# Optimization experiments

Measured on AMD Instinct MI355X. Metric: run time of the kernel, lower is better.

## Reference

```python
import jax, jax.numpy as jnp
import numpy as np

NUM_STEPS = 5  # matches init num_steps
N_NODES = 500_000
N_EDGES = 32_000_000


def setup_inputs() -> dict:
    key = jax.random.key(0)
    k1, k2, k3 = jax.random.split(key, 3)
    prior_probs = jax.random.uniform(k1, (N_NODES,), dtype=jnp.float32)
    edge_index = jax.random.randint(k2, (2, N_EDGES), 0, N_NODES, dtype=jnp.int32)
    edge_probs = jax.random.uniform(k3, (N_EDGES,), dtype=jnp.float32)
    return {"prior_probs": prior_probs, "edge_index": edge_index, "edge_probs": edge_probs}


def reference(prior_probs, edge_index, edge_probs):
    num_nodes = prior_probs.shape[0]
    source = edge_index[0]
    target = edge_index[1]
    p_t_u = prior_probs
    prod_terms = jnp.ones_like(prior_probs)
    for _ in range(NUM_STEPS):
        # gather node activation at source, weight by edge prob, scatter-add into target
        message = edge_probs * p_t_u[source]            # [E]
        agg = jax.ops.segment_sum(message, target, num_segments=num_nodes)  # [N]
        delta = 1.0 - jnp.exp(-agg)
        new_p_t_u = prod_terms * delta
        prod_terms = prod_terms * (1.0 - new_p_t_u)
        p_t_u = new_p_t_u
    p_final = 1.0 - prod_terms + prior_probs
    return p_final.reshape(-1, 1)
```

## Files before the change

### kernel.cpp

```cpp
#include <hip/hip_runtime.h>
#include <hip/hip_fp16.h>

#define NUM_STEPS 5
typedef unsigned int u32;

#define RSH 10
#define RSZ 1024
#define SB  512
#define ST  512
#define SPLIT 2
#define SRC_BITS 19
#define SRC_MASK 0x7FFFFu

static inline size_t align256(size_t x){ return (x + 255) & ~(size_t)255; }


__global__ void init_fast(const float* __restrict__ prior, __half* __restrict__ p,
                          float* __restrict__ prod, int n){
    int i = blockIdx.x*blockDim.x + threadIdx.x;
    if(i<n){ p[i]=__float2half_rn(prior[i]); prod[i]=1.0f; }
}

__global__ void hist_kernel(const int* __restrict__ dst, long long E, int B,
                            u32* __restrict__ blk_cnt){
    extern __shared__ u32 hist[];
    int sb = blockIdx.x;
    long long E4 = E >> 2;
    long long chunk = (E4 + SB - 1)/SB;
    long long i0 = (long long)sb*chunk;
    long long i1 = i0 + chunk; if(i1 > E4) i1 = E4;
    for(int b=threadIdx.x; b<B; b+=blockDim.x) hist[b]=0;
    __syncthreads();
    const int4* d4 = (const int4*)dst;
    for(long long i=i0+threadIdx.x; i<i1; i+=blockDim.x){
        int4 d = d4[i];
        atomicAdd(&hist[((u32)d.x)>>RSH], 1u);
        atomicAdd(&hist[((u32)d.y)>>RSH], 1u);
        atomicAdd(&hist[((u32)d.z)>>RSH], 1u);
        atomicAdd(&hist[((u32)d.w)>>RSH], 1u);
    }
    if(sb==0){
        for(long long e=(E4<<2)+threadIdx.x; e<E; e+=blockDim.x)
            atomicAdd(&hist[((u32)dst[e])>>RSH], 1u);
    }
    __syncthreads();
    for(int b=threadIdx.x; b<B; b+=blockDim.x) blk_cnt[(size_t)sb*B + b] = hist[b];
}

__global__ void colscan_kernel(u32* __restrict__ blk_cnt, int B, u32* __restrict__ tot){
    __shared__ u32 s[SB];
    int b = blockIdx.x, t = threadIdx.x;
    u32 v = blk_cnt[(size_t)t*B + b];
    s[t] = v; __syncthreads();
    for(int off=1; off<SB; off<<=1){
        u32 x = (t>=off) ? s[t-off] : 0;
        __syncthreads();
        s[t] += x;
        __syncthreads();
    }
    blk_cnt[(size_t)t*B + b] = s[t] - v;
    if(t==SB-1) tot[b] = s[SB-1];
}

__global__ void basescan_kernel(const u32* __restrict__ tot, u32* __restrict__ base, int B){
    __shared__ u32 s[256];
    int t = threadIdx.x;
    u32 v0 = (2*t   < B) ? tot[2*t]   : 0;
    u32 v1 = (2*t+1 < B) ? tot[2*t+1] : 0;
    u32 sum = v0 + v1;
    s[t] = sum; __syncthreads();
    for(int off=1; off<256; off<<=1){
        u32 x = (t>=off) ? s[t-off] : 0;
        __syncthreads();
        s[t] += x;
        __syncthreads();
    }
    u32 run = s[t] - sum;
    if(2*t   < B) base[2*t]   = run;
    if(2*t+1 < B) base[2*t+1] = run + v0;
    if(t==255) base[B] = s[255];
}

__global__ void scatter_kernel(const int* __restrict__ src, const int* __restrict__ dst,
                               const float* __restrict__ ep, long long E, int B,
                               const u32* __restrict__ blk_rel, const u32* __restrict__ base,
                               uint2* __restrict__ edges){
    extern __shared__ u32 cur[];
    int sb = blockIdx.x;
    long long E4 = E >> 2;
    long long chunk = (E4 + SB - 1)/SB;
    long long i0 = (long long)sb*chunk;
    long long i1 = i0 + chunk; if(i1 > E4) i1 = E4;
    for(int b=threadIdx.x; b<B; b+=blockDim.x)
        cur[b] = base[b] + blk_rel[(size_t)sb*B + b];
    __syncthreads();
    const int4*   s4 = (const int4*)src;
    const int4*   d4 = (const int4*)dst;
    const float4* w4 = (const float4*)ep;
    for(long long i=i0+threadIdx.x; i<i1; i+=blockDim.x){
        int4 s = s4[i]; int4 d = d4[i]; float4 w = w4[i];
        u32 dd, pos;
        dd=(u32)d.x; pos=atomicAdd(&cur[dd>>RSH],1u);
        edges[pos]=make_uint2(((u32)s.x)|((dd&(RSZ-1))<<SRC_BITS), __float_as_uint(w.x));
        dd=(u32)d.y; pos=atomicAdd(&cur[dd>>RSH],1u);
        edges[pos]=make_uint2(((u32)s.y)|((dd&(RSZ-1))<<SRC_BITS), __float_as_uint(w.y));
        dd=(u32)d.z; pos=atomicAdd(&cur[dd>>RSH],1u);
        edges[pos]=make_uint2(((u32)s.z)|((dd&(RSZ-1))<<SRC_BITS), __float_as_uint(w.z));
        dd=(u32)d.w; pos=atomicAdd(&cur[dd>>RSH],1u);
        edges[pos]=make_uint2(((u32)s.w)|((dd&(RSZ-1))<<SRC_BITS), __float_as_uint(w.w));
    }
    if(sb==0){
        for(long long e=(E4<<2)+threadIdx.x; e<E; e+=blockDim.x){
            u32 dd=(u32)dst[e];
            u32 pos=atomicAdd(&cur[dd>>RSH],1u);
            edges[pos]=make_uint2(((u32)src[e])|((dd&(RSZ-1))<<SRC_BITS), __float_as_uint(ep[e]));
        }
    }
}

__global__ __launch_bounds__(512) void
step_kernel(const uint2* __restrict__ edges, const u32* __restrict__ base,
            const __half* __restrict__ p, float* __restrict__ pacc){
    __shared__ float acc[2][RSZ];
    int blk = blockIdx.x;
    int b   = blk >> 1;
    int part= blk & 1;
    int t   = threadIdx.x;
    for(int k=t; k<RSZ; k+=blockDim.x){ acc[0][k]=0.0f; acc[1][k]=0.0f; }
    __syncthreads();
    u32 e0 = base[b], e1 = base[b+1];
    u32 cnt = e1 - e0;
    u32 s0 = e0 + (cnt*part)/SPLIT;
    u32 s1 = e0 + (cnt*(part+1))/SPLIT;
    int rep = t & 1;
    for(u32 e = s0 + t; e < s1; e += blockDim.x){
        uint2 pk = edges[e];
        float pv = __half2float(p[pk.x & SRC_MASK]);
        atomicAdd(&acc[rep][pk.x >> SRC_BITS], __uint_as_float(pk.y) * pv);
    }
    __syncthreads();
    float* dstp = pacc + (size_t)blk * RSZ;
    for(int k=t; k<RSZ; k+=blockDim.x) dstp[k] = acc[0][k] + acc[1][k];
}

__global__ void combine_kernel(const float* __restrict__ pacc, __half* __restrict__ p,
                               float* __restrict__ prod, const float* __restrict__ prior,
                               float* __restrict__ out, int n, int final_step){
    int i = blockIdx.x*blockDim.x + threadIdx.x;
    if(i < n){
        int b = i >> RSH, k = i & (RSZ-1);
        float a = pacc[(size_t)(b*SPLIT    )*RSZ + k]
                + pacc[(size_t)(b*SPLIT + 1)*RSZ + k];
        float pr_old = prod[i];
        float np = pr_old * (1.0f - expf(-a));
        float pr = pr_old * (1.0f - np);
        prod[i] = pr;
        p[i] = __float2half_rn(np);
        if(final_step) out[i] = 1.0f - pr + prior[i];
    }
}


__global__ void init_kernel(const float* __restrict__ prior, float* __restrict__ p,
                            float* __restrict__ prod, float* __restrict__ agg, int n){
    int i = blockIdx.x*blockDim.x + threadIdx.x;
    if(i<n){ p[i]=prior[i]; prod[i]=1.0f; agg[i]=0.0f; }
}

__global__ void edge_kernel(const int* __restrict__ src, const int* __restrict__ dst,
                            const float* __restrict__ ep, const float* __restrict__ p,
                            float* __restrict__ agg, int e4, int e_rem, long long e4base){
    int i = blockIdx.x*blockDim.x + threadIdx.x;
    if(i < e4){
        int4   s = ((const int4*)src)[i];
        int4   t = ((const int4*)dst)[i];
        float4 w = ((const float4*)ep)[i];
        atomicAdd(&agg[t.x], w.x * p[s.x]);
        atomicAdd(&agg[t.y], w.y * p[s.y]);
        atomicAdd(&agg[t.z], w.z * p[s.z]);
        atomicAdd(&agg[t.w], w.w * p[s.w]);
    }
    if(blockIdx.x==0 && threadIdx.x < e_rem){
        long long e = e4base + threadIdx.x;
        atomicAdd(&agg[dst[e]], ep[e]*p[src[e]]);
    }
}

__global__ void node_kernel(float* __restrict__ p, float* __restrict__ prod,
                            float* __restrict__ agg, const float* __restrict__ prior,
                            float* __restrict__ out, int n, int final_step){
    int i = blockIdx.x*blockDim.x + threadIdx.x;
    if(i<n){
        float a = agg[i]; agg[i]=0.0f;
        float pr_old = prod[i];
        float np = pr_old*(1.0f - expf(-a));
        float pr = pr_old*(1.0f - np);
        prod[i]=pr; p[i]=np;
        if(final_step) out[i] = 1.0f - pr + prior[i];
    }
}


extern "C" void kernel_launch(void* const* d_in, const int* in_sizes, int n_in,
                              void* d_out, int out_size, void* d_ws, size_t ws_size,
                              hipStream_t stream){
    const float* prior = (const float*)d_in[0];
    const int*   eidx  = (const int*)d_in[1];
    const float* ep    = (const float*)d_in[2];

    const int n = in_sizes[0];
    const long long E = (long long)in_sizes[2];
    const int* src = eidx;
    const int* dst = eidx + E;
    float* out = (float*)d_out;

    const int B = (n + RSZ - 1) >> RSH;

    size_t szNh  = align256((size_t)n * 2);
    size_t szN   = align256((size_t)n * 4);
    size_t szB1  = align256((size_t)(B + 1) * 4);
    size_t szB   = align256((size_t)B * 4);
    size_t szCnt = align256((size_t)SB * B * 4);
    size_t szAcc = align256((size_t)SPLIT * B * RSZ * 4);
    size_t szE2  = align256((size_t)E * 8);

    size_t off_p    = 0;
    size_t off_prod = off_p + szNh;
    size_t off_base = off_prod + szN;
    size_t off_tot  = off_base + szB1;
    size_t off_cnt  = off_tot + szB;
    size_t off_acc  = off_cnt + szCnt;
    size_t off_edge = off_acc + szAcc;
    size_t need     = off_edge + szE2;

    char* ws = (char*)d_ws;

    if(ws_size >= need && n < (1 << SRC_BITS) && B <= 512){
        __half* p    = (__half*)(ws + off_p);
        float*  prod = (float*) (ws + off_prod);
        u32*    base = (u32*)   (ws + off_base);
        u32*    tot  = (u32*)   (ws + off_tot);
        u32*    cnt  = (u32*)   (ws + off_cnt);
        float*  pacc = (float*) (ws + off_acc);
        uint2*  edges= (uint2*) (ws + off_edge);

        const int nb_n = (n + 255)/256;
        init_fast<<<nb_n, 256, 0, stream>>>(prior, p, prod, n);
        hist_kernel<<<SB, ST, (size_t)B*4, stream>>>(dst, E, B, cnt);
        colscan_kernel<<<B, SB, 0, stream>>>(cnt, B, tot);
        basescan_kernel<<<1, 256, 0, stream>>>(tot, base, B);
        scatter_kernel<<<SB, ST, (size_t)B*4, stream>>>(src, dst, ep, E, B, cnt, base, edges);

        for(int step=0; step<NUM_STEPS; ++step){
            step_kernel<<<B*SPLIT, 512, 0, stream>>>(edges, base, p, pacc);
            combine_kernel<<<nb_n, 256, 0, stream>>>(pacc, p, prod, prior, out, n,
                                                     step == NUM_STEPS-1 ? 1 : 0);
        }
    } else {
        float* p    = (float*)d_ws;
        float* prod = p + n;
        float* agg  = prod + n;
        const int nb_n = (n + 255)/256;
        init_kernel<<<nb_n, 256, 0, stream>>>(prior, p, prod, agg, n);
        const int e4 = (int)(E/4);
        const int e_rem = (int)(E%4);
        const long long e4base = (long long)e4*4;
        const int nb_e = (e4 + 255)/256;
        for(int step=0; step<NUM_STEPS; ++step){
            edge_kernel<<<nb_e, 256, 0, stream>>>(src, dst, ep, p, agg, e4, e_rem, e4base);
            node_kernel<<<nb_n, 256, 0, stream>>>(p, prod, agg, prior, out, n,
                                                  step == NUM_STEPS-1 ? 1 : 0);
        }
    }
}
```

Baseline: 1.346 ms.

## Stage scatter writes through shared-memory bins and unroll step kernel edge loop

The scatter kernel now buffers up to eight edges per destination bucket in shared memory and flushes full bins as contiguous 64-byte runs, so most global writes land as grouped stores instead of scattered 8-byte ones. Overflow edges past the bin capacity are written directly at their final slot. The step kernel loop is unrolled by four so several edge loads and gathers can be in flight before the LDS atomics. In exchange the scatter adds three block barriers per iteration and a larger static shared-memory footprint, which may lower occupancy.

```diff
diff --git a/kernel.cpp b/kernel.cpp
--- a/kernel.cpp
+++ b/kernel.cpp
@@ -7,7 +7,10 @@
 #define RSH 10
 #define RSZ 1024
 #define SB  512
+#define HT  512
 #define ST  512
+#define NBMAX 512
+#define BINS 8
 #define SPLIT 2
 #define SRC_BITS 19
 #define SRC_MASK 0x7FFFFu
@@ -81,40 +84,79 @@
     if(t==255) base[B] = s[255];
 }
 
-__global__ void scatter_kernel(const int* __restrict__ src, const int* __restrict__ dst,
-                               const float* __restrict__ ep, long long E, int B,
-                               const u32* __restrict__ blk_rel, const u32* __restrict__ base,
-                               uint2* __restrict__ edges){
-    extern __shared__ u32 cur[];
-    int sb = blockIdx.x;
+__global__ __launch_bounds__(ST) void
+scatter_kernel(const int* __restrict__ src, const int* __restrict__ dst,
+               const float* __restrict__ ep, long long E, int B,
+               const u32* __restrict__ blk_rel, const u32* __restrict__ base,
+               uint2* __restrict__ edges){
+    __shared__ uint2 bin[NBMAX][BINS];
+    __shared__ u32 cnt[NBMAX];
+    __shared__ u32 gcur[NBMAX];
+    const int sb = blockIdx.x, t = threadIdx.x;
     long long E4 = E >> 2;
     long long chunk = (E4 + SB - 1)/SB;
     long long i0 = (long long)sb*chunk;
     long long i1 = i0 + chunk; if(i1 > E4) i1 = E4;
-    for(int b=threadIdx.x; b<B; b+=blockDim.x)
-        cur[b] = base[b] + blk_rel[(size_t)sb*B + b];
-    __syncthreads();
-    const int4*   s4 = (const int4*)src;
-    const int4*   d4 = (const int4*)dst;
-    const float4* w4 = (const float4*)ep;
-    for(long long i=i0+threadIdx.x; i<i1; i+=blockDim.x){
-        int4 s = s4[i]; int4 d = d4[i]; float4 w = w4[i];
-        u32 dd, pos;
-        dd=(u32)d.x; pos=atomicAdd(&cur[dd>>RSH],1u);
-        edges[pos]=make_uint2(((u32)s.x)|((dd&(RSZ-1))<<SRC_BITS), __float_as_uint(w.x));
-        dd=(u32)d.y; pos=atomicAdd(&cur[dd>>RSH],1u);
-        edges[pos]=make_uint2(((u32)s.y)|((dd&(RSZ-1))<<SRC_BITS), __float_as_uint(w.y));
-        dd=(u32)d.z; pos=atomicAdd(&cur[dd>>RSH],1u);
-        edges[pos]=make_uint2(((u32)s.z)|((dd&(RSZ-1))<<SRC_BITS), __float_as_uint(w.z));
-        dd=(u32)d.w; pos=atomicAdd(&cur[dd>>RSH],1u);
-        edges[pos]=make_uint2(((u32)s.w)|((dd&(RSZ-1))<<SRC_BITS), __float_as_uint(w.w));
+    for(int b=t; b<B; b+=ST){ cnt[b]=0; gcur[b]=base[b]+blk_rel[(size_t)sb*B+b]; }
+    __syncthreads();
+    const int4*   s4=(const int4*)src;
+    const int4*   d4=(const int4*)dst;
+    const float4* w4=(const float4*)ep;
+    for(long long it=i0; it<i1; it+=ST){
+        long long i = it + t;
+        bool valid = (i < i1);
+        u32 bk[4]; u32 sl[4]; uint2 pl[4];
+        if(valid){
+            int4 s=s4[i]; int4 d=d4[i]; float4 w=w4[i];
+            u32 dd;
+            dd=(u32)d.x; bk[0]=dd>>RSH; pl[0]=make_uint2(((u32)s.x)|((dd&(RSZ-1))<<SRC_BITS), __float_as_uint(w.x));
+            dd=(u32)d.y; bk[1]=dd>>RSH; pl[1]=make_uint2(((u32)s.y)|((dd&(RSZ-1))<<SRC_BITS), __float_as_uint(w.y));
+            dd=(u32)d.z; bk[2]=dd>>RSH; pl[2]=make_uint2(((u32)s.z)|((dd&(RSZ-1))<<SRC_BITS), __float_as_uint(w.z));
+            dd=(u32)d.w; bk[3]=dd>>RSH; pl[3]=make_uint2(((u32)s.w)|((dd&(RSZ-1))<<SRC_BITS), __float_as_uint(w.w));
+            #pragma unroll
+            for(int k=0;k<4;k++) sl[k]=atomicAdd(&cnt[bk[k]],1u);
+        }
+        __syncthreads();
+        if(valid){
+            #pragma unroll
+            for(int k=0;k<4;k++){
+                if(sl[k] < BINS) bin[bk[k]][sl[k]] = pl[k];
+                else             edges[gcur[bk[k]] + sl[k]] = pl[k];
+            }
+        }
+        __syncthreads();
+        for(int b=t; b<B; b+=ST){
+            u32 c = cnt[b];
+            if(c >= BINS){
+                u32 g = gcur[b];
+                #pragma unroll
+                for(int k2=0;k2<BINS;k2++) edges[g+k2] = bin[b][k2];
+                gcur[b] = g + c;
+                cnt[b]  = 0;
+            }
+        }
+        __syncthreads();
     }
     if(sb==0){
-        for(long long e=(E4<<2)+threadIdx.x; e<E; e+=blockDim.x){
-            u32 dd=(u32)dst[e];
-            u32 pos=atomicAdd(&cur[dd>>RSH],1u);
-            edges[pos]=make_uint2(((u32)src[e])|((dd&(RSZ-1))<<SRC_BITS), __float_as_uint(ep[e]));
-        }
+        long long tb = E4<<2;
+        int nt = (int)(E - tb);
+        if(nt > 0){
+            bool v = (t < nt);
+            u32 bk0=0, sl0=0; uint2 pl0=make_uint2(0,0);
+            if(v){
+                u32 dd=(u32)dst[tb+t]; bk0=dd>>RSH;
+                pl0=make_uint2(((u32)src[tb+t])|((dd&(RSZ-1))<<SRC_BITS), __float_as_uint(ep[tb+t]));
+                sl0=atomicAdd(&cnt[bk0],1u);
+            }
+            __syncthreads();
+            if(v){ if(sl0<BINS) bin[bk0][sl0]=pl0; else edges[gcur[bk0]+sl0]=pl0; }
+            __syncthreads();
+        }
+    }
+    for(int b=t; b<B; b+=ST){
+        u32 c = cnt[b]; if(c > BINS) c = BINS;
+        u32 g = gcur[b];
+        for(u32 k2=0;k2<c;k2++) edges[g+k2] = bin[b][k2];
     }
 }
 
@@ -126,21 +168,39 @@
     int b   = blk >> 1;
     int part= blk & 1;
     int t   = threadIdx.x;
-    for(int k=t; k<RSZ; k+=blockDim.x){ acc[0][k]=0.0f; acc[1][k]=0.0f; }
+    for(int k=t; k<RSZ; k+=512){ acc[0][k]=0.0f; acc[1][k]=0.0f; }
     __syncthreads();
     u32 e0 = base[b], e1 = base[b+1];
     u32 cnt = e1 - e0;
-    u32 s0 = e0 + (cnt*part)/SPLIT;
-    u32 s1 = e0 + (cnt*(part+1))/SPLIT;
+    u32 s0 = e0 + (cnt*(u32)part)/SPLIT;
+    u32 s1 = e0 + (cnt*(u32)(part+1))/SPLIT;
     int rep = t & 1;
-    for(u32 e = s0 + t; e < s1; e += blockDim.x){
-        uint2 pk = edges[e];
-        float pv = __half2float(p[pk.x & SRC_MASK]);
-        atomicAdd(&acc[rep][pk.x >> SRC_BITS], __uint_as_float(pk.y) * pv);
+    u32 n = s1 - s0;
+    u32 m = n >> 11;
+    u32 eb = s0 + t;
+    for(u32 it=0; it<m; ++it){
+        uint2 a0 = edges[eb];
+        uint2 a1 = edges[eb+512];
+        uint2 a2 = edges[eb+1024];
+        uint2 a3 = edges[eb+1536];
+        float p0 = __half2float(p[a0.x & SRC_MASK]);
+        float p1 = __half2float(p[a1.x & SRC_MASK]);
+        float p2 = __half2float(p[a2.x & SRC_MASK]);
+        float p3 = __half2float(p[a3.x & SRC_MASK]);
+        atomicAdd(&acc[rep][a0.x >> SRC_BITS], __uint_as_float(a0.y)*p0);
+        atomicAdd(&acc[rep][a1.x >> SRC_BITS], __uint_as_float(a1.y)*p1);
+        atomicAdd(&acc[rep][a2.x >> SRC_BITS], __uint_as_float(a2.y)*p2);
+        atomicAdd(&acc[rep][a3.x >> SRC_BITS], __uint_as_float(a3.y)*p3);
+        eb += 2048;
+    }
+    for(u32 e=eb; e<s1; e+=512){
+        uint2 a = edges[e];
+        atomicAdd(&acc[rep][a.x >> SRC_BITS],
+                  __uint_as_float(a.y)*__half2float(p[a.x & SRC_MASK]));
     }
     __syncthreads();
     float* dstp = pacc + (size_t)blk * RSZ;
-    for(int k=t; k<RSZ; k+=blockDim.x) dstp[k] = acc[0][k] + acc[1][k];
+    for(int k=t; k<RSZ; k+=512) dstp[k] = acc[0][k] + acc[1][k];
 }
 
 __global__ void combine_kernel(const float* __restrict__ pacc, __half* __restrict__ p,
@@ -235,7 +295,7 @@
 
     char* ws = (char*)d_ws;
 
-    if(ws_size >= need && n < (1 << SRC_BITS) && B <= 512){
+    if(ws_size >= need && n < (1 << SRC_BITS) && B <= NBMAX){
         __half* p    = (__half*)(ws + off_p);
         float*  prod = (float*) (ws + off_prod);
         u32*    base = (u32*)   (ws + off_base);
@@ -246,10 +306,10 @@
 
         const int nb_n = (n + 255)/256;
         init_fast<<<nb_n, 256, 0, stream>>>(prior, p, prod, n);
-        hist_kernel<<<SB, ST, (size_t)B*4, stream>>>(dst, E, B, cnt);
+        hist_kernel<<<SB, HT, (size_t)B*4, stream>>>(dst, E, B, cnt);
         colscan_kernel<<<B, SB, 0, stream>>>(cnt, B, tot);
         basescan_kernel<<<1, 256, 0, stream>>>(tot, base, B);
-        scatter_kernel<<<SB, ST, (size_t)B*4, stream>>>(src, dst, ep, E, B, cnt, base, edges);
+        scatter_kernel<<<SB, ST, 0, stream>>>(src, dst, ep, E, B, cnt, base, edges);
 
         for(int step=0; step<NUM_STEPS; ++step){
             step_kernel<<<B*SPLIT, 512, 0, stream>>>(edges, base, p, pacc);
```

Result: faster. 1.162 ms (-13.6%).
